# Optimization experiments

Measured on AMD Instinct MI355X. Metric: run time of the kernel, lower is better.

Reference implementation:

```python
import jax, jax.numpy as jnp
import numpy as np

SIGMA = 0.05
KSIZE = 3
MIN_VAL = 50.0
MAX_VAL = 100.0


def _gauss_kernel():
    # ax = range(-(3//2)+1, 3//2+1) = [-1, 0, 1]  (matches TF int-floor-div)
    ax = jnp.arange(-(KSIZE // 2) + 1.0, KSIZE // 2 + 1.0)
    xx, yy = jnp.meshgrid(ax, ax)
    k = jnp.exp(-(xx ** 2 + yy ** 2) / (2.0 * SIGMA ** 2))
    k = k / jnp.sum(k)
    return k[..., None, None].astype(jnp.float32)  # HWIO, C=1


def _reflect_pad(x):
    return jnp.pad(x, ((0, 0), (1, 1), (1, 1), (0, 0)), mode='reflect')


def _conv(x, k):
    return jax.lax.conv_general_dilated(x, k, (1, 1), 'VALID',
                                        dimension_numbers=('NHWC', 'HWIO', 'NHWC'))


def _canny(images):
    blur = _conv(_reflect_pad(images), _gauss_kernel())
    h = jnp.array([[-1, 0, 1], [-2, 0, 2], [-1, 0, 1]], jnp.float32)[..., None, None]
    v = jnp.array([[-1, -2, -1], [0, 0, 0], [1, 2, 1]], jnp.float32)[..., None, None]
    bp = _reflect_pad(blur)
    gx = _conv(bp, h)
    gy = _conv(bp, v)
    gxy = jnp.sqrt(gx ** 2 + gy ** 2)
    # NOTE: original uses atan2(gx, gy) in this arg order
    theta = (jnp.arctan2(gx, gy) * (180.0 / np.pi) + 90.0) % 180.0

    H, W = gx.shape[1], gx.shape[2]
    # dilation2d with a -inf/0 kernel == max over the kernel's zero-offsets of the
    # zero-padded image; offsets are (dy,dx) of the 0 entries of each 3x3 filter.
    offsets = [
        [(1, 0), (1, 1), (1, 2)],  # horizontal bin: middle row
        [(0, 2), (1, 1), (2, 0)],  # 45 deg: anti-diagonal
        [(0, 1), (1, 1), (2, 1)],  # vertical bin: middle column
        [(0, 0), (1, 1), (2, 2)],  # 135 deg: main diagonal
    ]
    conds = [
        jnp.logical_or(theta >= 157.5, theta < 22.5),
        jnp.logical_and(theta >= 22.5, theta < 67.5),
        jnp.logical_and(theta >= 67.5, theta < 112.5),
        jnp.logical_and(theta >= 112.5, theta < 157.5),
    ]

    edge = jnp.zeros_like(gxy)
    for cond, offs in zip(conds, offsets):
        ang = jnp.where(cond, gxy, 0.0)
        pad = jnp.pad(ang, ((0, 0), (1, 1), (1, 1), (0, 0)))  # zero pad, as ZeroPadding2D
        mp = pad[:, offs[0][0]:offs[0][0] + H, offs[0][1]:offs[0][1] + W, :]
        for dy, dx in offs[1:]:
            mp = jnp.maximum(mp, pad[:, dy:dy + H, dx:dx + W, :])
        edge = edge + jnp.where(mp == ang, ang, 0.0)

    edge_sure = jnp.where(edge >= MAX_VAL, 255.0, 0.0)
    edge_week = jnp.where(jnp.logical_and(edge >= MIN_VAL, edge < MAX_VAL), 255.0, 0.0)
    edge_image = jnp.where(jnp.logical_or(edge_week == 255.0, edge_sure == 255.0), 255.5, 0.0)
    return edge_image, edge_week, edge_sure


def setup_inputs() -> dict:
    key = jax.random.key(0)
    images = jax.random.uniform(key, (16, 1024, 1024, 1), dtype=jnp.float32) * 255.0
    return {"images": images}


def reference(images):
    return _canny(images)
```

## Files before the change

kernel.cpp:

```cpp
#include <hip/hip_runtime.h>
#include <math.h>

#define IMG_H 1024
#define IMG_W 1024
#define OUT_H 1025
#define OUT_W 1025
#define NIMG  16
#define TOTAL (NIMG * OUT_H * OUT_W)

__device__ __forceinline__ int refl(int k) {
    if (k >= 2) return (k <= 1025) ? (k - 2) : 1022;
    return k;
}

__device__ __forceinline__ void sobel(const float* __restrict__ img, int i, int j,
                                      float& gx, float& gy) {
    int r0 = refl(i), r1 = refl(i + 1), r2 = refl(i + 2);
    int c0 = refl(j), c1 = refl(j + 1), c2 = refl(j + 2);
    const float* p0 = img + r0 * IMG_W;
    const float* p1 = img + r1 * IMG_W;
    const float* p2 = img + r2 * IMG_W;
    float v00 = p0[c0], v01 = p0[c1], v02 = p0[c2];
    float v10 = p1[c0],               v12 = p1[c2];
    float v20 = p2[c0], v21 = p2[c1], v22 = p2[c2];

    float t = -v00;
    t = __fadd_rn(t, v02);
    t = __fadd_rn(t, -2.0f * v10);
    t = __fadd_rn(t, 2.0f * v12);
    t = __fadd_rn(t, -v20);
    gx = __fadd_rn(t, v22);

    t = -v00;
    t = __fadd_rn(t, -2.0f * v01);
    t = __fadd_rn(t, -v02);
    t = __fadd_rn(t, v20);
    t = __fadd_rn(t, 2.0f * v21);
    gy = __fadd_rn(t, v22);
}

__device__ int classify_slow(float gx, float gy) {
    float t = (float)atan2((double)gx, (double)gy);
    float deg = __fmul_rn(t, (float)(180.0 / M_PI));
    float th = __fadd_rn(deg, 90.0f);
    th = fmodf(th, 180.0f);
    if (th < 0.0f) th += 180.0f;
    if (th < 22.5f || th >= 157.5f) return 0;
    if (th < 67.5f) return 1;
    if (th < 112.5f) return 2;
    return 3;
}

__device__ __forceinline__ int classify(float gx, float gy) {
    float ax = fabsf(gx), ay = fabsf(gy);
    const float T22_LO = 0.414172141e0f;
    const float T22_HI = 0.414254984e0f;
    const float T67_LO = 2.413972141e0f;
    const float T67_HI = 2.414454984e0f;

    if (ax <= ay * T22_LO) return 2;
    if (ax >= ay * T67_HI) return 0;
    if (ax >= ay * T22_HI && ax <= ay * T67_LO) {
        unsigned s = (__float_as_uint(gx) ^ __float_as_uint(gy)) >> 31;
        return s ? 1 : 3;
    }
    return classify_slow(gx, gy);
}

__device__ __forceinline__ float mag(float gx, float gy) {
    return __fsqrt_rn(__fadd_rn(__fmul_rn(gx, gx), __fmul_rn(gy, gy)));
}

__global__ __launch_bounds__(256) void canny_kernel(const float* __restrict__ images,
                                                    float* __restrict__ out) {
    int tid = blockIdx.x * 256 + threadIdx.x;
    if (tid >= TOTAL) return;

    int n   = tid / (OUT_H * OUT_W);
    int rem = tid % (OUT_H * OUT_W);
    int i = rem / OUT_W;
    int j = rem % OUT_W;

    const float* img = images + (size_t)n * IMG_H * IMG_W;

    float gxc, gyc;
    sobel(img, i, j, gxc, gyc);
    float gc = mag(gxc, gyc);
    int bc = classify(gxc, gyc);

    int di, dj;
    switch (bc) {
        case 0:  di = 0; dj = 1;  break;
        case 1:  di = 1; dj = -1; break;
        case 2:  di = 1; dj = 0;  break;
        default: di = 1; dj = 1;  break;
    }

    float nmax = 0.0f;
    int i1 = i + di, j1 = j + dj;
    if (i1 >= 0 && i1 < OUT_H && j1 >= 0 && j1 < OUT_W) {
        float gxn, gyn;
        sobel(img, i1, j1, gxn, gyn);
        if (classify(gxn, gyn) == bc) {
            float gn = mag(gxn, gyn);
            if (gn > nmax) nmax = gn;
        }
    }
    int i2 = i - di, j2 = j - dj;
    if (i2 >= 0 && i2 < OUT_H && j2 >= 0 && j2 < OUT_W) {
        float gxn, gyn;
        sobel(img, i2, j2, gxn, gyn);
        if (classify(gxn, gyn) == bc) {
            float gn = mag(gxn, gyn);
            if (gn > nmax) nmax = gn;
        }
    }

    float e = (gc >= nmax) ? gc : 0.0f;

    out[tid]             = (e >= 50.0f) ? 255.5f : 0.0f;
    out[TOTAL + tid]     = (e >= 50.0f && e < 100.0f) ? 255.0f : 0.0f;
    out[2 * TOTAL + tid] = (e >= 100.0f) ? 255.0f : 0.0f;
}

extern "C" void kernel_launch(void* const* d_in, const int* in_sizes, int n_in,
                              void* d_out, int out_size, void* d_ws, size_t ws_size,
                              hipStream_t stream) {
    const float* images = (const float*)d_in[0];
    float* out = (float*)d_out;
    int blocks = (TOTAL + 255) / 256;
    canny_kernel<<<blocks, 256, 0, stream>>>(images, out);
}
```

Measured before the change: 365.9 us.

## Compute gradient magnitude and direction bin once per tile in shared memory

Replaces per-pixel recomputation of Sobel gradients for the pixel and its two NMS neighbours with a tiled kernel. Each block first computes magnitude and direction bin for a 64x16 tile plus halo into shared memory, then performs non-maximum suppression from shared memory. This removes roughly threefold redundant gradient and classification work, at the cost of halo overhead, a block barrier and partially idle edge tiles.

```diff
diff --git a/kernel.cpp b/kernel.cpp
--- a/kernel.cpp
+++ b/kernel.cpp
@@ -7,6 +7,12 @@
 #define OUT_W 1025
 #define NIMG  16
 #define TOTAL (NIMG * OUT_H * OUT_W)
+
+#define TILE_W 64
+#define TILE_H 16
+#define HALO_W (TILE_W + 2)
+#define HALO_H (TILE_H + 2)
+#define NHALO  (HALO_W * HALO_H)
 
 __device__ __forceinline__ int refl(int k) {
     if (k >= 2) return (k <= 1025) ? (k - 2) : 1022;
@@ -73,54 +79,69 @@
 
 __global__ __launch_bounds__(256) void canny_kernel(const float* __restrict__ images,
                                                     float* __restrict__ out) {
-    int tid = blockIdx.x * 256 + threadIdx.x;
-    if (tid >= TOTAL) return;
+    __shared__ float         g_s[NHALO];
+    __shared__ unsigned char b_s[NHALO];
 
-    int n   = tid / (OUT_H * OUT_W);
-    int rem = tid % (OUT_H * OUT_W);
-    int i = rem / OUT_W;
-    int j = rem % OUT_W;
+    const int tile_ox = blockIdx.x * TILE_W;
+    const int tile_oy = blockIdx.y * TILE_H;
+    const int n       = blockIdx.z;
+    const float* img = images + (size_t)n * IMG_H * IMG_W;
+    const int t = threadIdx.x;
 
-    const float* img = images + (size_t)n * IMG_H * IMG_W;
+    for (int idx = t; idx < NHALO; idx += 256) {
+        int hy = idx / HALO_W;
+        int hx = idx - hy * HALO_W;
+        int oy = tile_oy + hy - 1;
+        int ox = tile_ox + hx - 1;
+        float g = -1.0f;
+        int   b = 255;
+        if (oy >= 0 && oy < OUT_H && ox >= 0 && ox < OUT_W) {
+            float gx, gy;
+            sobel(img, oy, ox, gx, gy);
+            g = mag(gx, gy);
+            b = classify(gx, gy);
+        }
+        g_s[idx] = g;
+        b_s[idx] = (unsigned char)b;
+    }
+    __syncthreads();
 
-    float gxc, gyc;
-    sobel(img, i, j, gxc, gyc);
-    float gc = mag(gxc, gyc);
-    int bc = classify(gxc, gyc);
+    const int col = t & (TILE_W - 1);
+    const int row0 = t >> 6;
+    const int ox = tile_ox + col;
+    if (ox >= OUT_W) return;
 
-    int di, dj;
-    switch (bc) {
-        case 0:  di = 0; dj = 1;  break;
-        case 1:  di = 1; dj = -1; break;
-        case 2:  di = 1; dj = 0;  break;
-        default: di = 1; dj = 1;  break;
+    #pragma unroll
+    for (int q = 0; q < 4; q++) {
+        int r = row0 + q * 4;
+        int oy = tile_oy + r;
+        if (oy >= OUT_H) continue;
+
+        int hc = (r + 1) * HALO_W + (col + 1);
+        float gc = g_s[hc];
+        int   bc = b_s[hc];
+
+        int doff;
+        switch (bc) {
+            case 0:  doff = 1;            break;
+            case 1:  doff = HALO_W - 1;   break;
+            case 2:  doff = HALO_W;       break;
+            default: doff = HALO_W + 1;   break;
+        }
+
+        float nmax = 0.0f;
+        float g1 = g_s[hc + doff];
+        if (b_s[hc + doff] == bc && g1 > nmax) nmax = g1;
+        float g2 = g_s[hc - doff];
+        if (b_s[hc - doff] == bc && g2 > nmax) nmax = g2;
+
+        float e = (gc >= nmax) ? gc : 0.0f;
+
+        size_t o = (size_t)(n * OUT_H + oy) * OUT_W + ox;
+        out[o]                       = (e >= 50.0f) ? 255.5f : 0.0f;
+        out[(size_t)TOTAL + o]       = (e >= 50.0f && e < 100.0f) ? 255.0f : 0.0f;
+        out[(size_t)(2 * TOTAL) + o] = (e >= 100.0f) ? 255.0f : 0.0f;
     }
-
-    float nmax = 0.0f;
-    int i1 = i + di, j1 = j + dj;
-    if (i1 >= 0 && i1 < OUT_H && j1 >= 0 && j1 < OUT_W) {
-        float gxn, gyn;
-        sobel(img, i1, j1, gxn, gyn);
-        if (classify(gxn, gyn) == bc) {
-            float gn = mag(gxn, gyn);
-            if (gn > nmax) nmax = gn;
-        }
-    }
-    int i2 = i - di, j2 = j - dj;
-    if (i2 >= 0 && i2 < OUT_H && j2 >= 0 && j2 < OUT_W) {
-        float gxn, gyn;
-        sobel(img, i2, j2, gxn, gyn);
-        if (classify(gxn, gyn) == bc) {
-            float gn = mag(gxn, gyn);
-            if (gn > nmax) nmax = gn;
-        }
-    }
-
-    float e = (gc >= nmax) ? gc : 0.0f;
-
-    out[tid]             = (e >= 50.0f) ? 255.5f : 0.0f;
-    out[TOTAL + tid]     = (e >= 50.0f && e < 100.0f) ? 255.0f : 0.0f;
-    out[2 * TOTAL + tid] = (e >= 100.0f) ? 255.0f : 0.0f;
 }
 
 extern "C" void kernel_launch(void* const* d_in, const int* in_sizes, int n_in,
@@ -128,6 +149,8 @@
                               hipStream_t stream) {
     const float* images = (const float*)d_in[0];
     float* out = (float*)d_out;
-    int blocks = (TOTAL + 255) / 256;
-    canny_kernel<<<blocks, 256, 0, stream>>>(images, out);
+    dim3 grid((OUT_W + TILE_W - 1) / TILE_W,
+              (OUT_H + TILE_H - 1) / TILE_H,
+              NIMG);
+    canny_kernel<<<grid, 256, 0, stream>>>(images, out);
 }
```

After: 315.5 us. -13.8%, faster.

## Restructure Canny into per-wave column strips with rolling rows and shuffle reuse

Applied to the files above, without the earlier changes.

Each wavefront processes a 60-column strip over a chunk of rows. It keeps a sliding 3-row window in registers and gets horizontal neighbours by lane shuffles, so each pixel's gradient, magnitude and angle class is computed once instead of up to three times. Classification becomes a mostly branchless path with a rare slow fallback. The cost is halo lanes that do no output work, fewer output columns per wave, and more complex edge fixup logic.

```diff
diff --git a/kernel.cpp b/kernel.cpp
--- a/kernel.cpp
+++ b/kernel.cpp
@@ -6,15 +6,23 @@
 #define OUT_H 1025
 #define OUT_W 1025
 #define NIMG  16
-#define TOTAL (NIMG * OUT_H * OUT_W)
+#define TOTAL ((size_t)NIMG * OUT_H * OUT_W)
+
+#define SW      60
+#define NSTRIP  18
+#define CHUNK   41
+#define NCHUNK  25
+#define WAVES_PER_IMG (NSTRIP * NCHUNK)
+#define TOTAL_WAVES   (NIMG * WAVES_PER_IMG)
+#define NTHREADS 128
 
 __device__ __forceinline__ int refl(int k) {
     if (k >= 2) return (k <= 1025) ? (k - 2) : 1022;
     return k;
 }
 
-__device__ __forceinline__ void sobel(const float* __restrict__ img, int i, int j,
-                                      float& gx, float& gy) {
+__device__ __forceinline__ void sobel_generic(const float* __restrict__ img, int i, int j,
+                                              float& gx, float& gy) {
     int r0 = refl(i), r1 = refl(i + 1), r2 = refl(i + 2);
     int c0 = refl(j), c1 = refl(j + 1), c2 = refl(j + 2);
     const float* p0 = img + r0 * IMG_W;
@@ -37,6 +45,25 @@
     t = __fadd_rn(t, v20);
     t = __fadd_rn(t, 2.0f * v21);
     gy = __fadd_rn(t, v22);
+}
+
+__device__ __forceinline__ void sobel9(float v00, float v01, float v02,
+                                       float v10, float v12,
+                                       float v20, float v21, float v22,
+                                       float& gx, float& gy) {
+    float s = -v00;
+    s = __fadd_rn(s, v02);
+    s = __fadd_rn(s, -2.0f * v10);
+    s = __fadd_rn(s, 2.0f * v12);
+    s = __fadd_rn(s, -v20);
+    gx = __fadd_rn(s, v22);
+
+    s = -v00;
+    s = __fadd_rn(s, -2.0f * v01);
+    s = __fadd_rn(s, -v02);
+    s = __fadd_rn(s, v20);
+    s = __fadd_rn(s, 2.0f * v21);
+    gy = __fadd_rn(s, v22);
 }
 
 __device__ int classify_slow(float gx, float gy) {
@@ -58,69 +85,127 @@
     const float T67_LO = 2.413972141e0f;
     const float T67_HI = 2.414454984e0f;
 
-    if (ax <= ay * T22_LO) return 2;
-    if (ax >= ay * T67_HI) return 0;
-    if (ax >= ay * T22_HI && ax <= ay * T67_LO) {
-        unsigned s = (__float_as_uint(gx) ^ __float_as_uint(gy)) >> 31;
-        return s ? 1 : 3;
-    }
-    return classify_slow(gx, gy);
+    bool in22 = (ax > ay * T22_LO) && (ax < ay * T22_HI);
+    bool in67 = (ax > ay * T67_LO) && (ax < ay * T67_HI);
+    if (__builtin_expect(in22 || in67, 0))
+        return classify_slow(gx, gy);
+
+    unsigned s = (__float_as_uint(gx) ^ __float_as_uint(gy)) >> 31;
+    int diag = s ? 1 : 3;
+    return (ax <= ay * T22_LO) ? 2 : ((ax >= ay * T67_HI) ? 0 : diag);
 }
 
 __device__ __forceinline__ float mag(float gx, float gy) {
     return __fsqrt_rn(__fadd_rn(__fmul_rn(gx, gx), __fmul_rn(gy, gy)));
 }
 
-__global__ __launch_bounds__(256) void canny_kernel(const float* __restrict__ images,
-                                                    float* __restrict__ out) {
-    int tid = blockIdx.x * 256 + threadIdx.x;
-    if (tid >= TOTAL) return;
-
-    int n   = tid / (OUT_H * OUT_W);
-    int rem = tid % (OUT_H * OUT_W);
-    int i = rem / OUT_W;
-    int j = rem % OUT_W;
-
-    const float* img = images + (size_t)n * IMG_H * IMG_W;
-
-    float gxc, gyc;
-    sobel(img, i, j, gxc, gyc);
-    float gc = mag(gxc, gyc);
-    int bc = classify(gxc, gyc);
-
-    int di, dj;
-    switch (bc) {
-        case 0:  di = 0; dj = 1;  break;
-        case 1:  di = 1; dj = -1; break;
-        case 2:  di = 1; dj = 0;  break;
-        default: di = 1; dj = 1;  break;
+__global__ __launch_bounds__(NTHREADS, 8) void canny_kernel(const float* __restrict__ images,
+                                                            float* __restrict__ out) {
+    const int wid  = blockIdx.x * (NTHREADS / 64) + (threadIdx.x >> 6);
+    const int lane = threadIdx.x & 63;
+    const int n    = wid / WAVES_PER_IMG;
+    const int rem  = wid - n * WAVES_PER_IMG;
+    const int s    = rem / NCHUNK;
+    const int k    = rem - s * NCHUNK;
+
+    const float* img = images + (size_t)n * (IMG_H * IMG_W);
+    const int gc0  = s * SW - 1;
+    const int gcol = gc0 + lane;
+    const int Y0   = k * CHUNK;
+
+    int lc = gcol - 2;
+    lc = lc < 0 ? 0 : (lc > 1023 ? 1023 : lc);
+
+    const bool gv      = (lane <= 61) && (gcol >= 0) && (gcol <= 1024);
+    const bool needfix = gv && (gcol <= 1 || gcol == 1024);
+    const bool ov      = (lane >= 1) && (lane <= 60) && (gcol <= 1024);
+
+    float AL, AC, AR, BL, BC, BR, CL, CC, CR, pend;
+
+    #define LDROW(mr) (img[(mr) * IMG_W + lc])
+    #define SHUF(L, C, R) do { C = __shfl_down(L, 1); R = __shfl_down(L, 2); } while (0)
+
+    #define COMPUTE_G(rg, gdst, bdst) do {                                   \
+        float _gx, _gy;                                                      \
+        sobel9(AL, AC, AR, BL, BR, CL, CC, CR, _gx, _gy);                    \
+        if (needfix) sobel_generic(img, (rg), gcol, _gx, _gy);               \
+        gdst = mag(_gx, _gy);                                                \
+        bdst = (unsigned)classify(_gx, _gy);                                 \
+        if (!gv) { gdst = 0.0f; bdst = 255u; }                               \
+    } while (0)
+
+    float gm1v, g0v, gp1v;
+    unsigned bm1, b0, bp1;
+
+    if (k == 0) {
+        AL = LDROW(0); SHUF(AL, AC, AR);
+        BL = LDROW(1); SHUF(BL, BC, BR);
+        CL = AL; CC = AC; CR = AR;
+        COMPUTE_G(0, g0v, b0);
+        gm1v = 0.0f; bm1 = 255u;
+    } else {
+        int r0 = Y0 - 1;
+        AL = LDROW(r0 - 2); SHUF(AL, AC, AR);
+        BL = LDROW(r0 - 1); SHUF(BL, BC, BR);
+        CL = LDROW(r0);     SHUF(CL, CC, CR);
+        COMPUTE_G(r0, gm1v, bm1);
+        AL = BL; AC = BC; AR = BR;  BL = CL; BC = CC; BR = CR;
+        CL = LDROW(refl(r0 + 3)); SHUF(CL, CC, CR);
+        COMPUTE_G(Y0, g0v, b0);
     }
-
-    float nmax = 0.0f;
-    int i1 = i + di, j1 = j + dj;
-    if (i1 >= 0 && i1 < OUT_H && j1 >= 0 && j1 < OUT_W) {
-        float gxn, gyn;
-        sobel(img, i1, j1, gxn, gyn);
-        if (classify(gxn, gyn) == bc) {
-            float gn = mag(gxn, gyn);
-            if (gn > nmax) nmax = gn;
+    {
+        int pr = Y0 + 3; pr = pr > 1026 ? 1026 : pr;
+        pend = LDROW(refl(pr));
+    }
+
+    float* const out_i = out;
+    float* const out_w = out + TOTAL;
+    float* const out_s = out + 2 * TOTAL;
+    int o = (n * OUT_H + Y0) * OUT_W + gcol;
+
+    for (int y = Y0; y < Y0 + CHUNK; ++y) {
+        int yn = y + 1;
+        if (yn <= 1024) {
+            AL = BL; AC = BC; AR = BR;  BL = CL; BC = CC; BR = CR;
+            CL = pend; SHUF(CL, CC, CR);
+            int pr = y + 4; pr = pr > 1026 ? 1026 : pr;
+            pend = LDROW(refl(pr));
+            COMPUTE_G(yn, gp1v, bp1);
+        } else {
+            gp1v = 0.0f; bp1 = 255u;
         }
+
+        unsigned pk  = bm1 | (b0 << 8) | (bp1 << 16);
+        float g0E = __shfl_down(g0v, 1),  g0W = __shfl_up(g0v, 1);
+        float gmE = __shfl_down(gm1v, 1), gmW = __shfl_up(gm1v, 1);
+        float gpE = __shfl_down(gp1v, 1), gpW = __shfl_up(gp1v, 1);
+        unsigned pkE = (unsigned)__shfl_down((int)pk, 1);
+        unsigned pkW = (unsigned)__shfl_up((int)pk, 1);
+
+        unsigned bc = b0;
+        float    n1 = bc == 0 ? g0E : (bc == 1 ? gpW : (bc == 2 ? gp1v : gpE));
+        unsigned q1 = bc == 0 ? pkE : (bc == 1 ? pkW : (bc == 2 ? pk  : pkE));
+        unsigned s1 = bc == 0 ? ((q1 >> 8) & 255u) : ((q1 >> 16) & 255u);
+        float    n2 = bc == 0 ? g0W : (bc == 1 ? gmE : (bc == 2 ? gm1v : gmW));
+        unsigned q2 = bc == 0 ? pkW : (bc == 1 ? pkE : (bc == 2 ? pk  : pkW));
+        unsigned s2 = bc == 0 ? ((q2 >> 8) & 255u) : (q2 & 255u);
+
+        float m1 = (s1 == bc) ? n1 : 0.0f;
+        float m2 = (s2 == bc) ? n2 : 0.0f;
+        float mx = fmaxf(m1, m2);
+        float e  = (g0v >= mx) ? g0v : 0.0f;
+
+        if (ov) {
+            out_i[o] = (e >= 50.0f) ? 255.5f : 0.0f;
+            out_w[o] = (e >= 50.0f && e < 100.0f) ? 255.0f : 0.0f;
+            out_s[o] = (e >= 100.0f) ? 255.0f : 0.0f;
+        }
+        o += OUT_W;
+        gm1v = g0v; bm1 = b0;  g0v = gp1v; b0 = bp1;
     }
-    int i2 = i - di, j2 = j - dj;
-    if (i2 >= 0 && i2 < OUT_H && j2 >= 0 && j2 < OUT_W) {
-        float gxn, gyn;
-        sobel(img, i2, j2, gxn, gyn);
-        if (classify(gxn, gyn) == bc) {
-            float gn = mag(gxn, gyn);
-            if (gn > nmax) nmax = gn;
-        }
-    }
-
-    float e = (gc >= nmax) ? gc : 0.0f;
-
-    out[tid]             = (e >= 50.0f) ? 255.5f : 0.0f;
-    out[TOTAL + tid]     = (e >= 50.0f && e < 100.0f) ? 255.0f : 0.0f;
-    out[2 * TOTAL + tid] = (e >= 100.0f) ? 255.0f : 0.0f;
+    #undef LDROW
+    #undef SHUF
+    #undef COMPUTE_G
 }
 
 extern "C" void kernel_launch(void* const* d_in, const int* in_sizes, int n_in,
@@ -128,6 +213,6 @@
                               hipStream_t stream) {
     const float* images = (const float*)d_in[0];
     float* out = (float*)d_out;
-    int blocks = (TOTAL + 255) / 256;
-    canny_kernel<<<blocks, 256, 0, stream>>>(images, out);
-}
+    int blocks = TOTAL_WAVES / (NTHREADS / 64);
+    canny_kernel<<<blocks, NTHREADS, 0, stream>>>(images, out);
+}
```

Result: faster. 355.3 us (-2.9%).
